# Kernel optimization log

Measured on AMD Instinct MI355X. Metric: run time of the kernel, lower is better.

The kernel has to match this reference:

```python
import jax, jax.numpy as jnp
import numpy as np

S, B, H, V, U = 512, 16, 256, 10000, 10000
LAMBDA_T = 0.1   # flashback default temporal decay
LAMBDA_S = 100.0 # flashback default spatial decay
DAY = 86400.0


def setup_inputs() -> dict:
    key = jax.random.key(0)
    ks = jax.random.split(key, 16)
    x = jax.random.randint(ks[0], (S, B), 0, V)
    t = jax.random.uniform(ks[1], (S, B), jnp.float32) * (7.0 * DAY)  # timestamps in seconds
    s = jax.random.normal(ks[2], (S, B, 2), jnp.float32)              # lat/lon-like coords
    y_t = jax.random.uniform(ks[3], (S, B), jnp.float32)
    y_s = jax.random.normal(ks[4], (S, B, 2), jnp.float32)
    h = jnp.zeros((2, B, H), jnp.float32)
    active_user = jax.random.randint(ks[5], (1, B), 0, U)
    sc = 0.02
    enc_emb = jax.random.normal(ks[6], (V, H), jnp.float32) * sc
    user_emb = jax.random.normal(ks[7], (U, H), jnp.float32) * sc
    Wih_f = jax.random.normal(ks[8], (H, H), jnp.float32) * sc
    Whh_f = jax.random.normal(ks[9], (H, H), jnp.float32) * sc
    b_f = jnp.zeros((H,), jnp.float32)
    Wih_b = jax.random.normal(ks[10], (H, H), jnp.float32) * sc
    Whh_b = jax.random.normal(ks[11], (H, H), jnp.float32) * sc
    b_b = jnp.zeros((H,), jnp.float32)
    fc_W = jax.random.normal(ks[12], (V, 3 * H), jnp.float32) * sc
    fc_b = jnp.zeros((V,), jnp.float32)
    return dict(x=x, t=t, s=s, y_t=y_t, y_s=y_s, h=h, active_user=active_user,
                enc_emb=enc_emb, user_emb=user_emb,
                Wih_f=Wih_f, Whh_f=Whh_f, b_f=b_f,
                Wih_b=Wih_b, Whh_b=Whh_b, b_b=b_b,
                fc_W=fc_W, fc_b=fc_b)


def _rnn_dir(xe, h0, Wih, Whh, b):
    # vanilla tanh RNN over leading (time) axis; xe: [S,B,H]
    def step(hprev, xt):
        hn = jnp.tanh(xt @ Wih.T + hprev @ Whh.T + b)
        return hn, hn
    hT, ys = jax.lax.scan(step, h0, xe)
    return ys, hT


def _forward(x, t, s, h, active_user, enc_emb, user_emb,
             Wih_f, Whh_f, b_f, Wih_b, Whh_b, b_b, fc_W, fc_b):
    seq_len, user_len = x.shape
    x_emb = enc_emb[x]                           # [S,B,H]
    out_f, h_f = _rnn_dir(x_emb, h[0], Wih_f, Whh_f, b_f)
    out_b_rev, h_b = _rnn_dir(x_emb[::-1], h[1], Wih_b, Whh_b, b_b)
    h_out = jnp.stack([h_f, h_b], 0)             # [2,B,H]

    # pairwise causal decay weights (i = query step, j = key step, j <= i)
    dt = t[:, None, :] - t[None, :, :]           # [S,S,B]
    ds = jnp.sqrt(jnp.sum((s[:, None] - s[None, :]) ** 2, axis=-1))  # [S,S,B]
    a = ((jnp.cos(dt * (2.0 * np.pi / DAY)) + 1.0) * 0.5) * jnp.exp(-(dt / DAY) * LAMBDA_T)
    b_w = jnp.exp(-ds * LAMBDA_S)
    w = a * b_w + 1e-10                          # [S,S,B]
    causal = jnp.tril(jnp.ones((seq_len, seq_len), w.dtype))
    w = w * causal[:, :, None]
    sum_w = jnp.sum(w, axis=1)                   # [S,B]
    out_w_forward = jnp.einsum('ijb,jbh->ibh', w, out_f) / sum_w[:, :, None]
    # NOTE: original code has a bug (accumulates out_w_backward into itself),
    # so out_w_backward is identically zero; reproduce faithfully.
    out_w_backward = jnp.zeros_like(out_w_forward)

    out_w = jnp.concatenate([out_w_forward, out_w_backward], axis=2)  # [S,B,2H]
    ow = jnp.transpose(out_w, (1, 0, 2))         # [B,S,2H]
    # dropout is identity in eval mode -> query == out_w
    scores = jnp.einsum('bqd,bkd->bqk', ow, ow) / jnp.sqrt(jnp.asarray(2 * H, ow.dtype))
    alpha = jax.nn.softmax(scores, axis=-1)
    ctx = jnp.einsum('bqk,bkd->bqd', alpha, ow)  # [B,S,2H]
    attn_output = jnp.transpose(ctx, (1, 0, 2))  # [S,B,2H]

    p_u = user_emb[active_user.reshape(user_len)]            # [B,H]
    p_u_b = jnp.broadcast_to(p_u[None], (seq_len, user_len, H))
    out_pu = jnp.concatenate([attn_output, p_u_b], axis=2)   # [S,B,3H]
    y_linear = out_pu @ fc_W.T + fc_b                        # [S,B,V]
    return y_linear, h_out


def reference(x, t, s, y_t, y_s, h, active_user, enc_emb, user_emb,
              Wih_f, Whh_f, b_f, Wih_b, Whh_b, b_b, fc_W, fc_b):
    return _forward(x, t, s, h, active_user, enc_emb, user_emb,
                    Wih_f, Whh_f, b_f, Wih_b, Whh_b, b_b, fc_W, fc_b)
```

## Files before the change

kernel.cpp:

```cpp
#include <hip/hip_runtime.h>

typedef unsigned short ushort_t;
typedef __attribute__((ext_vector_type(8))) short short8;
typedef __attribute__((ext_vector_type(4))) float f32x4;

#define S_LEN 512
#define NB 16
#define NH 256
#define NV 10000

__device__ __forceinline__ unsigned short f2bf(float f){
  unsigned u = __float_as_uint(f);
  u += 0x7fffu + ((u >> 16) & 1u);
  return (unsigned short)(u >> 16);
}

__global__ __launch_bounds__(512) void k_prep0(const int* __restrict__ x,
    const float* __restrict__ emb, ushort_t* __restrict__ xe, ushort_t* __restrict__ xer,
    const float* __restrict__ WihF, ushort_t* __restrict__ wihf,
    const float* __restrict__ WihB, ushort_t* __restrict__ wihb){
  int bx = blockIdx.x, tid = threadIdx.x;
  if (bx < 512){
    int g = bx * 512 + tid;
    int m = g >> 5, c = (g & 31) << 3;
    int xm = x[m];
    const float* src = emb + (size_t)xm * NH + c;
    float4 a = *(const float4*)src, b = *(const float4*)(src + 4);
    union { ushort_t us[8]; uint4 v; } u;
    u.us[0]=f2bf(a.x); u.us[1]=f2bf(a.y); u.us[2]=f2bf(a.z); u.us[3]=f2bf(a.w);
    u.us[4]=f2bf(b.x); u.us[5]=f2bf(b.y); u.us[6]=f2bf(b.z); u.us[7]=f2bf(b.w);
    int s = m >> 4, bidx = m & 15;
    int mr = ((S_LEN - 1 - s) << 4) | bidx;
    *(uint4*)&xe [(size_t)m  * NH + c] = u.v;
    *(uint4*)&xer[(size_t)mr * NH + c] = u.v;
    return;
  }
  bx -= 512;
  const float* src = (bx < 16) ? WihF : WihB;
  ushort_t* dst = (bx < 16) ? wihf : wihb;
  int g = ((bx & 15) * 512 + tid) * 8;
  float4 a = *(const float4*)(src + g), b = *(const float4*)(src + g + 4);
  union { ushort_t us[8]; uint4 v; } u;
  u.us[0]=f2bf(a.x); u.us[1]=f2bf(a.y); u.us[2]=f2bf(a.z); u.us[3]=f2bf(a.w);
  u.us[4]=f2bf(b.x); u.us[5]=f2bf(b.y); u.us[6]=f2bf(b.z); u.us[7]=f2bf(b.w);
  *(uint4*)&dst[g] = u.v;
}

__global__ __launch_bounds__(256) void k_transpose(const ushort_t* __restrict__ src,
    ushort_t* __restrict__ dst, int R, int C, long long sstride, long long dstride){
  __shared__ ushort_t tile[32][33];
  int z = blockIdx.z;
  int c0 = blockIdx.x * 32, r0 = blockIdx.y * 32;
  int tx = threadIdx.x & 31, ty = threadIdx.x >> 5;
  const ushort_t* Sp = src + (size_t)sstride * z;
  ushort_t* Dp = dst + (size_t)dstride * z;
  #pragma unroll
  for (int i = 0; i < 32; i += 8) tile[ty+i][tx] = Sp[(size_t)(r0+ty+i) * C + c0 + tx];
  __syncthreads();
  #pragma unroll
  for (int i = 0; i < 32; i += 8) Dp[(size_t)(c0+ty+i) * R + r0 + tx] = tile[tx][ty+i];
}

__global__ __launch_bounds__(256, 2) void k_gemm(
    const ushort_t* __restrict__ A, const ushort_t* __restrict__ Bt, void* __restrict__ Cp,
    int M, int N, int K, int lda, int ldb, int ldc,
    long long sAz, long long sBz, long long sCz,
    const float* __restrict__ bias,
    const float* __restrict__ rowscale, int rsStride,
    const float* __restrict__ addrow, int ldu,
    float cscale, int cmode){
  __shared__ __align__(16) ushort_t As[128 * 40];
  __shared__ __align__(16) ushort_t Bs[128 * 40];
  int z = blockIdx.z;
  int n0 = blockIdx.x * 128, m0 = blockIdx.y * 128;
  int tid = threadIdx.x;
  int wave = tid >> 6, lane = tid & 63;
  int l15 = lane & 15, q4 = lane >> 4;
  int wm = (wave >> 1) * 64, wn = (wave & 1) * 64;
  const ushort_t* Ab = A + (size_t)sAz * z;
  const ushort_t* Bb = Bt + (size_t)sBz * z;
  int srow = tid >> 1, scol = (tid & 1) * 16;
  f32x4 acc[4][4];
  #pragma unroll
  for (int tm = 0; tm < 4; tm++)
    #pragma unroll
    for (int tn = 0; tn < 4; tn++) acc[tm][tn] = (f32x4){0.f,0.f,0.f,0.f};

  for (int k0 = 0; k0 < K; k0 += 32){
    __syncthreads();
    const ushort_t* ap = Ab + (size_t)(m0+srow)*lda + k0 + scol;
    const ushort_t* bp = Bb + (size_t)(n0+srow)*ldb + k0 + scol;
    *(uint4*)&As[srow*40 + scol]     = *(const uint4*)ap;
    *(uint4*)&As[srow*40 + scol + 8] = *(const uint4*)(ap + 8);
    *(uint4*)&Bs[srow*40 + scol]     = *(const uint4*)bp;
    *(uint4*)&Bs[srow*40 + scol + 8] = *(const uint4*)(bp + 8);
    __syncthreads();
    short8 af[4], bf[4];
    #pragma unroll
    for (int tm = 0; tm < 4; tm++) af[tm] = *(const short8*)&As[(wm + tm*16 + l15)*40 + q4*8];
    #pragma unroll
    for (int tn = 0; tn < 4; tn++) bf[tn] = *(const short8*)&Bs[(wn + tn*16 + l15)*40 + q4*8];
    #pragma unroll
    for (int tm = 0; tm < 4; tm++)
      #pragma unroll
      for (int tn = 0; tn < 4; tn++)
        acc[tm][tn] = __builtin_amdgcn_mfma_f32_16x16x32_bf16(af[tm], bf[tn], acc[tm][tn], 0, 0, 0);
  }

  #pragma unroll
  for (int tm = 0; tm < 4; tm++)
    #pragma unroll
    for (int tn = 0; tn < 4; tn++)
      #pragma unroll
      for (int r = 0; r < 4; r++){
        int mr = m0 + wm + tm*16 + q4*4 + r;
        int nc = n0 + wn + tn*16 + l15;
        if (nc < N && mr < M){
          float v = acc[tm][tn][r] * cscale;
          if (bias)     v += bias[nc];
          if (rowscale) v *= rowscale[(size_t)z * rsStride + mr];
          if (addrow)   v += addrow[(size_t)(mr & 15) * ldu + nc];
          if (cmode == 0){
            ((float*)Cp)[(size_t)sCz * z + (size_t)mr * ldc + nc] = v;
          } else if (cmode == 1){
            ((ushort_t*)Cp)[(size_t)sCz * z + (size_t)mr * ldc + nc] = f2bf(v);
          } else {
            ((ushort_t*)Cp)[((size_t)mr * 16 + z) * ldc + nc] = f2bf(v);
          }
        }
      }
}

__global__ __launch_bounds__(512, 1) void k_fused(
    const float* __restrict__ WhhF, const float* __restrict__ WhhB,
    const float* __restrict__ xWf, const float* __restrict__ xWb,
    const float* __restrict__ h0,
    ushort_t* __restrict__ outf,
    float* __restrict__ hout,
    const float* __restrict__ fcW, ushort_t* __restrict__ fcw1, ushort_t* __restrict__ fcw2,
    const float* __restrict__ t, const float* __restrict__ s2,
    ushort_t* __restrict__ wb, float* __restrict__ rsum,
    const int* __restrict__ au, const float* __restrict__ uemb, ushort_t* __restrict__ pu){
  __shared__ __align__(16) ushort_t hl[2][8 * 264];
  int bx = blockIdx.x, tid = threadIdx.x;

  if (bx >= 4){
    int pb = bx - 4;
    if (pb < 632){
      int g = pb * 512 + tid;
      int v = g >> 5, c = (g & 31) << 3;
      union { ushort_t us[8]; uint4 q; } u1, u2;
      if (v < NV){
        const float* p1 = fcW + (size_t)v * 768 + c;
        const float* p2 = p1 + 512;
        float4 a1 = *(const float4*)p1, b1 = *(const float4*)(p1 + 4);
        float4 a2 = *(const float4*)p2, b2 = *(const float4*)(p2 + 4);
        u1.us[0]=f2bf(a1.x); u1.us[1]=f2bf(a1.y); u1.us[2]=f2bf(a1.z); u1.us[3]=f2bf(a1.w);
        u1.us[4]=f2bf(b1.x); u1.us[5]=f2bf(b1.y); u1.us[6]=f2bf(b1.z); u1.us[7]=f2bf(b1.w);
        u2.us[0]=f2bf(a2.x); u2.us[1]=f2bf(a2.y); u2.us[2]=f2bf(a2.z); u2.us[3]=f2bf(a2.w);
        u2.us[4]=f2bf(b2.x); u2.us[5]=f2bf(b2.y); u2.us[6]=f2bf(b2.z); u2.us[7]=f2bf(b2.w);
      } else {
        u1.q = make_uint4(0,0,0,0); u2.q = u1.q;
      }
      *(uint4*)&fcw1[(size_t)v * NH + c] = u1.q;
      *(uint4*)&fcw2[(size_t)v * NH + c] = u2.q;
      return;
    }
    pb -= 632;
    if (pb < 8192){
      float* red = (float*)hl;
      int i = pb >> 4, b = pb & 15, j = tid;
      const float C1 = 7.272205216643040e-05f;
      const float C2 = -1.1574074074074074e-06f;
      float ti  = t[i*16 + b];
      float sxi = s2[(size_t)(i*16 + b) * 2], syi = s2[(size_t)(i*16 + b) * 2 + 1];
      float w = 0.f;
      if (j <= i){
        float dt = ti - t[j*16 + b];
        float dx = sxi - s2[(size_t)(j*16 + b) * 2];
        float dy = syi - s2[(size_t)(j*16 + b) * 2 + 1];
        float ds = sqrtf(dx*dx + dy*dy);
        float a = (__cosf(dt * C1) + 1.f) * 0.5f * __expf(dt * C2);
        float bw = __expf(-100.f * ds);
        w = a * bw + 1e-10f;
      }
      wb[((size_t)b * S_LEN + i) * S_LEN + j] = f2bf(w);
      red[j] = w; __syncthreads();
      for (int st = 256; st > 0; st >>= 1){
        if (j < st) red[j] += red[j + st];
        __syncthreads();
      }
      if (j == 0) rsum[b * S_LEN + i] = 1.f / red[0];
      return;
    }
    pb -= 8192;
    int g = pb * 512 + tid;
    int r = g >> 5, c = (g & 31) << 3;
    union { ushort_t us[8]; uint4 q; } u;
    if (r < 16){
      const float* p = uemb + (size_t)au[r] * NH + c;
      float4 a = *(const float4*)p, b2 = *(const float4*)(p + 4);
      u.us[0]=f2bf(a.x); u.us[1]=f2bf(a.y); u.us[2]=f2bf(a.z); u.us[3]=f2bf(a.w);
      u.us[4]=f2bf(b2.x); u.us[5]=f2bf(b2.y); u.us[6]=f2bf(b2.z); u.us[7]=f2bf(b2.w);
    } else {
      u.q = make_uint4(0,0,0,0);
    }
    *(uint4*)&pu[(size_t)r * NH + c] = u.q;
    return;
  }

  int dir = bx >> 1, half = bx & 1;
  const float* Whh = dir ? WhhB : WhhF;
  const float* xW  = dir ? xWb : xWf;
  int wave = tid >> 6, lane = tid & 63;
  int l15 = lane & 15, q4 = lane >> 4;

  for (int idx = tid; idx < 2048; idx += 512){
    int m = idx >> 8, n = idx & 255;
    hl[0][m*264 + n] = f2bf(h0[((size_t)dir * 16 + half * 8 + m) * NH + n]);
  }

  short8 bfr[2][8];
  #pragma unroll
  for (int tn = 0; tn < 2; tn++)
    #pragma unroll
    for (int kk = 0; kk < 8; kk++){
      int n = wave*32 + tn*16 + l15;
      int k = kk*32 + q4*8;
      const float* wp = Whh + (size_t)n * NH + k;
      float4 wa = *(const float4*)wp, wb2 = *(const float4*)(wp + 4);
      short8 f;
      f[0]=(short)f2bf(wa.x); f[1]=(short)f2bf(wa.y); f[2]=(short)f2bf(wa.z); f[3]=(short)f2bf(wa.w);
      f[4]=(short)f2bf(wb2.x); f[5]=(short)f2bf(wb2.y); f[6]=(short)f2bf(wb2.z); f[7]=(short)f2bf(wb2.w);
      bfr[tn][kk] = f;
    }

  int myTn = q4 >> 1;
  int mb   = (q4 & 1) * 4;
  int ncol = wave*32 + myTn*16 + l15;

  const float* xwp = xW + (size_t)(half*8 + mb) * NH + ncol;
  float xwE[4], xwO[4];
  #pragma unroll
  for (int r = 0; r < 4; r++){
    xwE[r] = xwp[r * 256];
    xwO[r] = xwp[r * 256 + 16 * 256];
  }
  xwp += 2 * 16 * 256;

  ushort_t* outp0 = outf + (size_t)(half*8 + mb) * 512 * NH + ncol;
  ushort_t* outp1 = outp0 + (size_t)512 * NH;
  ushort_t* outp2 = outp1 + (size_t)512 * NH;
  ushort_t* outp3 = outp2 + (size_t)512 * NH;

  __builtin_amdgcn_s_setprio(1);
  __syncthreads();

#define RNN_STEP(S_, RB_, WB_, XWU_)                                              \
  {                                                                               \
    short8 af[8];                                                                 \
    _Pragma("unroll")                                                             \
    for (int kk = 0; kk < 8; kk++)                                                \
      af[kk] = *(const short8*)&hl[RB_][(lane & 7)*264 + kk*32 + q4*8];           \
    f32x4 a0a = (f32x4){0.f,0.f,0.f,0.f}, a0b = a0a, a1a = a0a, a1b = a0a;        \
    _Pragma("unroll")                                                             \
    for (int kk = 0; kk < 4; kk++){                                               \
      a0a = __builtin_amdgcn_mfma_f32_16x16x32_bf16(af[kk], bfr[0][kk], a0a, 0,0,0); \
      a1a = __builtin_amdgcn_mfma_f32_16x16x32_bf16(af[kk], bfr[1][kk], a1a, 0,0,0); \
    }                                                                             \
    _Pragma("unroll")                                                             \
    for (int kk = 4; kk < 8; kk++){                                               \
      a0b = __builtin_amdgcn_mfma_f32_16x16x32_bf16(af[kk], bfr[0][kk], a0b, 0,0,0); \
      a1b = __builtin_amdgcn_mfma_f32_16x16x32_bf16(af[kk], bfr[1][kk], a1b, 0,0,0); \
    }                                                                             \
    f32x4 accS = myTn ? (a1a + a1b) : (a0a + a0b);                                \
    float hv[4];                                                                  \
    _Pragma("unroll")                                                             \
    for (int r = 0; r < 4; r++){                                                  \
      float pre = accS[r] + XWU_[r];                                              \
      float ex = __expf(2.f * pre);                                               \
      hv[r] = 1.f - 2.f * __builtin_amdgcn_rcpf(ex + 1.f);                        \
      hl[WB_][(mb + r)*264 + ncol] = f2bf(hv[r]);                                 \
    }                                                                             \
    if (dir == 0){                                                                \
      outp0[0] = f2bf(hv[0]); outp1[0] = f2bf(hv[1]);                             \
      outp2[0] = f2bf(hv[2]); outp3[0] = f2bf(hv[3]);                             \
      outp0 += 256; outp1 += 256; outp2 += 256; outp3 += 256;                     \
    }                                                                             \
    if ((S_) == 511){                                                             \
      _Pragma("unroll")                                                           \
      for (int r = 0; r < 4; r++)                                                 \
        hout[((size_t)dir*16 + half*8 + mb + r) * NH + ncol] = hv[r];             \
    }                                                                             \
    if ((S_) < 510){                                                              \
      _Pragma("unroll")                                                           \
      for (int r = 0; r < 4; r++) XWU_[r] = xwp[r * 256];                         \
      xwp += 16 * 256;                                                            \
    }                                                                             \
    asm volatile("s_waitcnt lgkmcnt(0)" ::: "memory");                            \
    __builtin_amdgcn_s_barrier();                                                 \
    asm volatile("" ::: "memory");                                                \
  }

  for (int s = 0; s < 512; s += 2){
    RNN_STEP(s,     0, 1, xwE)
    RNN_STEP(s + 1, 1, 0, xwO)
  }
#undef RNN_STEP
}

__global__ __launch_bounds__(256) void k_softmax(const float* __restrict__ sc,
                                                 ushort_t* __restrict__ alpha){
  int q = blockIdx.x, z = blockIdx.y, tid = threadIdx.x;
  const float* row = sc + ((size_t)z * S_LEN + q) * S_LEN;
  float v0 = row[tid], v1 = row[tid + 256];
  __shared__ float red[256];
  red[tid] = fmaxf(v0, v1); __syncthreads();
  for (int st = 128; st > 0; st >>= 1){
    if (tid < st) red[tid] = fmaxf(red[tid], red[tid + st]);
    __syncthreads();
  }
  float mx = red[0]; __syncthreads();
  float e0 = __expf(v0 - mx), e1 = __expf(v1 - mx);
  red[tid] = e0 + e1; __syncthreads();
  for (int st = 128; st > 0; st >>= 1){
    if (tid < st) red[tid] += red[tid + st];
    __syncthreads();
  }
  float inv = 1.f / red[0];
  ushort_t* arow = alpha + ((size_t)z * S_LEN + q) * S_LEN;
  arow[tid]       = f2bf(e0 * inv);
  arow[tid + 256] = f2bf(e1 * inv);
}

extern "C" void kernel_launch(void* const* d_in, const int* in_sizes, int n_in,
                              void* d_out, int out_size, void* d_ws, size_t ws_size,
                              hipStream_t stream){
  const int*   x    = (const int*)d_in[0];
  const float* t    = (const float*)d_in[1];
  const float* s2   = (const float*)d_in[2];
  const float* h0   = (const float*)d_in[5];
  const int*   au   = (const int*)d_in[6];
  const float* emb  = (const float*)d_in[7];
  const float* uemb = (const float*)d_in[8];
  const float* WihF = (const float*)d_in[9];
  const float* WhhF = (const float*)d_in[10];
  const float* bF   = (const float*)d_in[11];
  const float* WihB = (const float*)d_in[12];
  const float* WhhB = (const float*)d_in[13];
  const float* bB   = (const float*)d_in[14];
  const float* fcW  = (const float*)d_in[15];
  const float* fcb  = (const float*)d_in[16];
  float* y    = (float*)d_out;
  float* hout = y + (size_t)S_LEN * NB * NV;

  char* wsc = (char*)d_ws;
  size_t off = 0;
  auto alloc = [&](size_t bytes) -> void* {
    void* p = wsc + off;
    off += (bytes + 255) & ~(size_t)255;
    return p;
  };
  ushort_t* xe    = (ushort_t*)alloc(8192 * 256 * 2);
  ushort_t* xer   = (ushort_t*)alloc(8192 * 256 * 2);
  ushort_t* wihf  = (ushort_t*)alloc(256 * 256 * 2);
  ushort_t* wihb  = (ushort_t*)alloc(256 * 256 * 2);
  float*    xwf   = (float*)alloc((size_t)8192 * 256 * 4);
  float*    xwb   = (float*)alloc((size_t)8192 * 256 * 4);
  ushort_t* outf  = (ushort_t*)alloc((size_t)16 * 512 * 256 * 2);
  ushort_t* outfT = (ushort_t*)alloc((size_t)16 * 256 * 512 * 2);
  ushort_t* wbuf  = (ushort_t*)alloc((size_t)16 * 512 * 512 * 2);
  float*    rsum  = (float*)alloc(16 * 512 * 4);
  ushort_t* owf   = (ushort_t*)alloc((size_t)16 * 512 * 256 * 2);
  ushort_t* owfT  = (ushort_t*)alloc((size_t)16 * 256 * 512 * 2);
  ushort_t* fcw1  = (ushort_t*)alloc((size_t)10112 * 256 * 2);
  float*    ulog  = (float*)alloc((size_t)16 * NV * 4);
  ushort_t* ctx   = (ushort_t*)alloc((size_t)8192 * 256 * 2);
  float*    scores = xwf;
  ushort_t* alpha  = wbuf;
  ushort_t* fcw2 = xe;
  ushort_t* pu   = wihf;

  k_prep0<<<dim3(544), dim3(512), 0, stream>>>(x, emb, xe, xer, WihF, wihf, WihB, wihb);

  k_gemm<<<dim3(2, 64, 1), dim3(256), 0, stream>>>(xe, wihf, xwf,
      8192, 256, 256, 256, 256, 256, 0, 0, 0, bF, nullptr, 0, nullptr, 0, 1.f, 0);
  k_gemm<<<dim3(2, 64, 1), dim3(256), 0, stream>>>(xer, wihb, xwb,
      8192, 256, 256, 256, 256, 256, 0, 0, 0, bB, nullptr, 0, nullptr, 0, 1.f, 0);

  k_fused<<<dim3(4 + 632 + 8192 + 8), dim3(512), 0, stream>>>(
      WhhF, WhhB, xwf, xwb, h0, outf, hout,
      fcW, fcw1, fcw2, t, s2, wbuf, rsum, au, uemb, pu);

  k_gemm<<<dim3(79, 1, 1), dim3(256), 0, stream>>>(pu, fcw2, ulog,
      16, NV, 256, 256, 256, NV, 0, 0, 0, fcb, nullptr, 0, nullptr, 0, 1.f, 0);

  k_transpose<<<dim3(8, 16, 16), dim3(256), 0, stream>>>(outf, outfT, 512, 256,
      (long long)512 * 256, (long long)256 * 512);

  k_gemm<<<dim3(2, 4, 16), dim3(256), 0, stream>>>(wbuf, outfT, owf,
      512, 256, 512, 512, 512, 256,
      (long long)512 * 512, (long long)256 * 512, (long long)512 * 256,
      nullptr, rsum, 512, nullptr, 0, 1.f, 1);
  k_transpose<<<dim3(8, 16, 16), dim3(256), 0, stream>>>(owf, owfT, 512, 256,
      (long long)512 * 256, (long long)256 * 512);

  k_gemm<<<dim3(4, 4, 16), dim3(256), 0, stream>>>(owf, owf, scores,
      512, 512, 256, 256, 256, 512,
      (long long)512 * 256, (long long)512 * 256, (long long)512 * 512,
      nullptr, nullptr, 0, nullptr, 0, 0.04419417382415922f, 0);

  k_softmax<<<dim3(512, 16), dim3(256), 0, stream>>>(scores, alpha);

  k_gemm<<<dim3(2, 4, 16), dim3(256), 0, stream>>>(alpha, owfT, ctx,
      512, 256, 512, 512, 512, 256,
      (long long)512 * 512, (long long)256 * 512, 0,
      nullptr, nullptr, 0, nullptr, 0, 1.f, 2);

  k_gemm<<<dim3(79, 64, 1), dim3(256), 0, stream>>>(ctx, fcw1, y,
      8192, 10000, 256, 256, 256, 10000, 0, 0, 0,
      nullptr, nullptr, 0, ulog, 10000, 1.f, 0);
}
```

Before: 942.8 us.

## Fuse attention scores, softmax and context into one flash-style kernel

Replaces the scores GEMM, the standalone softmax kernel and the alpha·V GEMM with a single online-softmax attention kernel. Each wave keeps 16 query rows in registers, streams key tiles from global memory, rescales running max and sum, and stages probabilities in LDS for the PV MFMAs. This removes the fp32 scores and bf16 alpha round trips through memory and two launches. Separately, the forward and backward input-projection GEMMs are merged into one z-batched launch, using a concatenated bias buffer and the contiguous workspace layout. The fused kernel launches only 64 blocks and reads K/V from global memory without LDS sharing, so it may leave much of the GPU idle.

```diff
diff --git a/kernel.cpp b/kernel.cpp
--- a/kernel.cpp
+++ b/kernel.cpp
@@ -18,7 +18,9 @@
 __global__ __launch_bounds__(512) void k_prep0(const int* __restrict__ x,
     const float* __restrict__ emb, ushort_t* __restrict__ xe, ushort_t* __restrict__ xer,
     const float* __restrict__ WihF, ushort_t* __restrict__ wihf,
-    const float* __restrict__ WihB, ushort_t* __restrict__ wihb){
+    const float* __restrict__ WihB, ushort_t* __restrict__ wihb,
+    const float* __restrict__ bF, const float* __restrict__ bB,
+    float* __restrict__ biascat){
   int bx = blockIdx.x, tid = threadIdx.x;
   if (bx < 512){
     int g = bx * 512 + tid;
@@ -35,6 +37,10 @@
     *(uint4*)&xer[(size_t)mr * NH + c] = u.v;
     return;
   }
+  if (bx == 544){
+    biascat[tid] = (tid < 256) ? bF[tid] : bB[tid - 256];
+    return;
+  }
   bx -= 512;
   const float* src = (bx < 16) ? WihF : WihB;
   ushort_t* dst = (bx < 16) ? wihf : wihb;
@@ -65,7 +71,7 @@
     const ushort_t* __restrict__ A, const ushort_t* __restrict__ Bt, void* __restrict__ Cp,
     int M, int N, int K, int lda, int ldb, int ldc,
     long long sAz, long long sBz, long long sCz,
-    const float* __restrict__ bias,
+    const float* __restrict__ bias, int biasZ,
     const float* __restrict__ rowscale, int rsStride,
     const float* __restrict__ addrow, int ldu,
     float cscale, int cmode){
@@ -117,7 +123,7 @@
         int nc = n0 + wn + tn*16 + l15;
         if (nc < N && mr < M){
           float v = acc[tm][tn][r] * cscale;
-          if (bias)     v += bias[nc];
+          if (bias)     v += bias[nc + z * biasZ];
           if (rowscale) v *= rowscale[(size_t)z * rsStride + mr];
           if (addrow)   v += addrow[(size_t)(mr & 15) * ldu + nc];
           if (cmode == 0){
@@ -309,28 +315,112 @@
 #undef RNN_STEP
 }
 
-__global__ __launch_bounds__(256) void k_softmax(const float* __restrict__ sc,
-                                                 ushort_t* __restrict__ alpha){
-  int q = blockIdx.x, z = blockIdx.y, tid = threadIdx.x;
-  const float* row = sc + ((size_t)z * S_LEN + q) * S_LEN;
-  float v0 = row[tid], v1 = row[tid + 256];
-  __shared__ float red[256];
-  red[tid] = fmaxf(v0, v1); __syncthreads();
-  for (int st = 128; st > 0; st >>= 1){
-    if (tid < st) red[tid] = fmaxf(red[tid], red[tid + st]);
-    __syncthreads();
-  }
-  float mx = red[0]; __syncthreads();
-  float e0 = __expf(v0 - mx), e1 = __expf(v1 - mx);
-  red[tid] = e0 + e1; __syncthreads();
-  for (int st = 128; st > 0; st >>= 1){
-    if (tid < st) red[tid] += red[tid + st];
-    __syncthreads();
-  }
-  float inv = 1.f / red[0];
-  ushort_t* arow = alpha + ((size_t)z * S_LEN + q) * S_LEN;
-  arow[tid]       = f2bf(e0 * inv);
-  arow[tid + 256] = f2bf(e1 * inv);
+__global__ __launch_bounds__(512, 1) void k_attn(
+    const ushort_t* __restrict__ owf,
+    const ushort_t* __restrict__ owfT,
+    ushort_t* __restrict__ ctx){
+  int qt = blockIdx.x, b = blockIdx.y;
+  int tid = threadIdx.x, wave = tid >> 6, lane = tid & 63;
+  int l15 = lane & 15, q4 = lane >> 4;
+  const ushort_t* ob  = owf  + (size_t)b * 512 * 256;
+  const ushort_t* otb = owfT + (size_t)b * 256 * 512;
+  __shared__ __align__(16) ushort_t pball[8][16 * 136];
+  ushort_t* pb = pball[wave];
+  int qrow = qt * 128 + wave * 16;
+
+  short8 aq[8];
+  #pragma unroll
+  for (int kc = 0; kc < 8; kc++)
+    aq[kc] = *(const short8*)&ob[(size_t)(qrow + l15) * 256 + kc*32 + q4*8];
+
+  const float sc = 0.04419417382415922f;
+  float m_run[4], l_run[4];
+  #pragma unroll
+  for (int r = 0; r < 4; r++){ m_run[r] = -3.0e38f; l_run[r] = 0.f; }
+  f32x4 cacc[16];
+  #pragma unroll
+  for (int hn = 0; hn < 16; hn++) cacc[hn] = (f32x4){0.f,0.f,0.f,0.f};
+
+  for (int kt = 0; kt < 4; kt++){
+    f32x4 sacc[8];
+    #pragma unroll
+    for (int n = 0; n < 8; n++) sacc[n] = (f32x4){0.f,0.f,0.f,0.f};
+    #pragma unroll
+    for (int kc = 0; kc < 8; kc++){
+      #pragma unroll
+      for (int n = 0; n < 8; n++){
+        short8 bk = *(const short8*)&ob[(size_t)(kt*128 + n*16 + l15) * 256 + kc*32 + q4*8];
+        sacc[n] = __builtin_amdgcn_mfma_f32_16x16x32_bf16(aq[kc], bk, sacc[n], 0, 0, 0);
+      }
+    }
+    #pragma unroll
+    for (int n = 0; n < 8; n++)
+      #pragma unroll
+      for (int r = 0; r < 4; r++) sacc[n][r] *= sc;
+
+    float tmax[4];
+    #pragma unroll
+    for (int r = 0; r < 4; r++){
+      float mx = sacc[0][r];
+      #pragma unroll
+      for (int n = 1; n < 8; n++) mx = fmaxf(mx, sacc[n][r]);
+      tmax[r] = mx;
+    }
+    #pragma unroll
+    for (int mk = 1; mk < 16; mk <<= 1)
+      #pragma unroll
+      for (int r = 0; r < 4; r++) tmax[r] = fmaxf(tmax[r], __shfl_xor(tmax[r], mk));
+    float mnew[4], resc[4], psum[4];
+    #pragma unroll
+    for (int r = 0; r < 4; r++){
+      mnew[r] = fmaxf(m_run[r], tmax[r]);
+      resc[r] = __expf(m_run[r] - mnew[r]);
+      m_run[r] = mnew[r];
+      psum[r] = 0.f;
+    }
+    #pragma unroll
+    for (int n = 0; n < 8; n++)
+      #pragma unroll
+      for (int r = 0; r < 4; r++){
+        float p = __expf(sacc[n][r] - mnew[r]);
+        psum[r] += p;
+        pb[(q4*4 + r)*136 + n*16 + l15] = f2bf(p);
+      }
+    #pragma unroll
+    for (int mk = 1; mk < 16; mk <<= 1)
+      #pragma unroll
+      for (int r = 0; r < 4; r++) psum[r] += __shfl_xor(psum[r], mk);
+    #pragma unroll
+    for (int r = 0; r < 4; r++) l_run[r] = l_run[r] * resc[r] + psum[r];
+    #pragma unroll
+    for (int hn = 0; hn < 16; hn++)
+      #pragma unroll
+      for (int r = 0; r < 4; r++) cacc[hn][r] *= resc[r];
+
+    asm volatile("s_waitcnt lgkmcnt(0)" ::: "memory");
+    __builtin_amdgcn_sched_barrier(0);
+
+    #pragma unroll
+    for (int kc2 = 0; kc2 < 4; kc2++){
+      short8 ap = *(const short8*)&pb[l15*136 + kc2*32 + q4*8];
+      #pragma unroll
+      for (int hn = 0; hn < 16; hn++){
+        short8 bv = *(const short8*)&otb[(size_t)(hn*16 + l15) * 512 + kt*128 + kc2*32 + q4*8];
+        cacc[hn] = __builtin_amdgcn_mfma_f32_16x16x32_bf16(ap, bv, cacc[hn], 0, 0, 0);
+      }
+    }
+  }
+
+  float inv[4];
+  #pragma unroll
+  for (int r = 0; r < 4; r++) inv[r] = 1.f / l_run[r];
+  #pragma unroll
+  for (int hn = 0; hn < 16; hn++)
+    #pragma unroll
+    for (int r = 0; r < 4; r++){
+      int q = qrow + q4*4 + r;
+      ctx[((size_t)q * 16 + b) * 256 + hn*16 + l15] = f2bf(cacc[hn][r] * inv[r]);
+    }
 }
 
 extern "C" void kernel_launch(void* const* d_in, const int* in_sizes, int n_in,
@@ -375,25 +465,25 @@
   ushort_t* owfT  = (ushort_t*)alloc((size_t)16 * 256 * 512 * 2);
   ushort_t* fcw1  = (ushort_t*)alloc((size_t)10112 * 256 * 2);
   float*    ulog  = (float*)alloc((size_t)16 * NV * 4);
+  float*    biascat = (float*)alloc(512 * 4);
   ushort_t* ctx   = (ushort_t*)alloc((size_t)8192 * 256 * 2);
-  float*    scores = xwf;
-  ushort_t* alpha  = wbuf;
   ushort_t* fcw2 = xe;
   ushort_t* pu   = wihf;
 
-  k_prep0<<<dim3(544), dim3(512), 0, stream>>>(x, emb, xe, xer, WihF, wihf, WihB, wihb);
-
-  k_gemm<<<dim3(2, 64, 1), dim3(256), 0, stream>>>(xe, wihf, xwf,
-      8192, 256, 256, 256, 256, 256, 0, 0, 0, bF, nullptr, 0, nullptr, 0, 1.f, 0);
-  k_gemm<<<dim3(2, 64, 1), dim3(256), 0, stream>>>(xer, wihb, xwb,
-      8192, 256, 256, 256, 256, 256, 0, 0, 0, bB, nullptr, 0, nullptr, 0, 1.f, 0);
+  k_prep0<<<dim3(545), dim3(512), 0, stream>>>(x, emb, xe, xer, WihF, wihf, WihB, wihb,
+                                               bF, bB, biascat);
+
+  k_gemm<<<dim3(2, 64, 2), dim3(256), 0, stream>>>(xe, wihf, xwf,
+      8192, 256, 256, 256, 256, 256,
+      (long long)8192 * 256, (long long)256 * 256, (long long)8192 * 256,
+      biascat, 256, nullptr, 0, nullptr, 0, 1.f, 0);
 
   k_fused<<<dim3(4 + 632 + 8192 + 8), dim3(512), 0, stream>>>(
       WhhF, WhhB, xwf, xwb, h0, outf, hout,
       fcW, fcw1, fcw2, t, s2, wbuf, rsum, au, uemb, pu);
 
   k_gemm<<<dim3(79, 1, 1), dim3(256), 0, stream>>>(pu, fcw2, ulog,
-      16, NV, 256, 256, 256, NV, 0, 0, 0, fcb, nullptr, 0, nullptr, 0, 1.f, 0);
+      16, NV, 256, 256, 256, NV, 0, 0, 0, fcb, 0, nullptr, 0, nullptr, 0, 1.f, 0);
 
   k_transpose<<<dim3(8, 16, 16), dim3(256), 0, stream>>>(outf, outfT, 512, 256,
       (long long)512 * 256, (long long)256 * 512);
@@ -401,23 +491,13 @@
   k_gemm<<<dim3(2, 4, 16), dim3(256), 0, stream>>>(wbuf, outfT, owf,
       512, 256, 512, 512, 512, 256,
       (long long)512 * 512, (long long)256 * 512, (long long)512 * 256,
-      nullptr, rsum, 512, nullptr, 0, 1.f, 1);
+      nullptr, 0, rsum, 512, nullptr, 0, 1.f, 1);
   k_transpose<<<dim3(8, 16, 16), dim3(256), 0, stream>>>(owf, owfT, 512, 256,
       (long long)512 * 256, (long long)256 * 512);
 
-  k_gemm<<<dim3(4, 4, 16), dim3(256), 0, stream>>>(owf, owf, scores,
-      512, 512, 256, 256, 256, 512,
-      (long long)512 * 256, (long long)512 * 256, (long long)512 * 512,
-      nullptr, nullptr, 0, nullptr, 0, 0.04419417382415922f, 0);
-
-  k_softmax<<<dim3(512, 16), dim3(256), 0, stream>>>(scores, alpha);
-
-  k_gemm<<<dim3(2, 4, 16), dim3(256), 0, stream>>>(alpha, owfT, ctx,
-      512, 256, 512, 512, 512, 256,
-      (long long)512 * 512, (long long)256 * 512, 0,
-      nullptr, nullptr, 0, nullptr, 0, 1.f, 2);
+  k_attn<<<dim3(4, 16), dim3(512), 0, stream>>>(owf, owfT, ctx);
 
   k_gemm<<<dim3(79, 64, 1), dim3(256), 0, stream>>>(ctx, fcw1, y,
       8192, 10000, 256, 256, 256, 10000, 0, 0, 0,
-      nullptr, nullptr, 0, ulog, 10000, 1.f, 0);
-}
+      nullptr, 0, nullptr, 0, ulog, 10000, 1.f, 0);
+}
```

After: 1.018 ms. +8.0%, slower.
